# Kernel tuning notes

Hardware: AMD Instinct MI355X
Metric: run time of the kernel (lower is better)

Reference implementation:

```python
import jax, jax.numpy as jnp
import numpy as np

SMILE_LEN = 40


def _gru_cell(x, h, Wih, Whh, bih, bhh):
    # PyTorch GRU gate order: r, z, n
    gi = x @ Wih.T + bih          # [B, 3H]
    gh = h @ Whh.T + bhh          # [B, 3H]
    H = h.shape[-1]
    ir, iz, inn = gi[:, :H], gi[:, H:2 * H], gi[:, 2 * H:]
    hr, hz, hn = gh[:, :H], gh[:, H:2 * H], gh[:, 2 * H:]
    r = jax.nn.sigmoid(ir + hr)
    z = jax.nn.sigmoid(iz + hz)
    n = jnp.tanh(inn + r * hn)
    return (1.0 - z) * n + z * h


def setup_inputs() -> dict:
    key = jax.random.key(0)
    ks = jax.random.split(key, 12)
    B, L, H, A = 16384, 128, 256, 21
    s = 0.05
    return {
        "latent": jax.random.normal(ks[0], (B, L), jnp.float32),
        "W1": jax.random.normal(ks[1], (H, L), jnp.float32) * s,
        "b1": jax.random.normal(ks[2], (H,), jnp.float32) * s,
        "W2": jax.random.normal(ks[3], (H, H), jnp.float32) * s,
        "b2": jax.random.normal(ks[4], (H,), jnp.float32) * s,
        "Wih": jax.random.normal(ks[5], (3 * H, A), jnp.float32) * s,
        "Whh": jax.random.normal(ks[6], (3 * H, H), jnp.float32) * s,
        "bih": jax.random.normal(ks[7], (3 * H,), jnp.float32) * s,
        "bhh": jax.random.normal(ks[8], (3 * H,), jnp.float32) * s,
        "Wd": jax.random.normal(ks[9], (A, H), jnp.float32) * s,
        "bd": jax.random.normal(ks[10], (A,), jnp.float32) * s,
    }


def reference(latent, W1, b1, W2, b2, Wih, Whh, bih, bhh, Wd, bd):
    B = latent.shape[0]
    A = Wih.shape[1]
    # latent -> Dense -> ReLU -> (Dropout: identity in eval) -> Dense
    hidden = jax.nn.relu(latent @ W1.T + b1) @ W2.T + b2  # [B, H]
    # start token: +32 at position 0, -32 elsewhere
    start = jnp.full((B, A), -32.0, jnp.float32).at[:, 0].set(32.0)

    def step(carry, _):
        h, inp = carry
        h_new = _gru_cell(inp, h, Wih, Whh, bih, bhh)
        pred = h_new @ Wd.T + bd                      # [B, A]
        return (h_new, jax.lax.stop_gradient(pred)), pred

    (_, _), preds = jax.lax.scan(step, (hidden, start), None, length=SMILE_LEN - 1)
    # preds: [T-1, B, A] -> y: [B, T, A] with start token at t=0
    y = jnp.concatenate([start[:, None, :], jnp.transpose(preds, (1, 0, 2))], axis=1)
    return y
```

## Files before the change

kernel.cpp:

```cpp
#include <hip/hip_runtime.h>
#include <hip/hip_bf16.h>


typedef __bf16 bf16x8 __attribute__((ext_vector_type(8)));
typedef float  f32x16 __attribute__((ext_vector_type(16)));

#define MFMA32(a,b,c) __builtin_amdgcn_mfma_f32_32x32x16_bf16((a),(b),(c),0,0,0)

static constexpr int A_DIM = 21;

static constexpr size_t O_W1F   = 0;
static constexpr size_t O_W2F   = O_W1F  + 256*128*2;
static constexpr size_t O_WHHF  = O_W2F  + 256*256*2;
static constexpr size_t O_WMF   = O_WHHF + 768*256*2;
static constexpr size_t O_WDF   = O_WMF  + 1024*256*2;
static constexpr size_t O_BMAIN = O_WDF  + 32*256*2;
static constexpr size_t O_GI1   = O_BMAIN + 1024*4;


__global__ void prep_frag(const float* __restrict__ src, __bf16* __restrict__ dst,
                          int SR, int SC, int NF, int NCH) {
  int total = NF * NCH * 512;
  for (int i = blockIdx.x * blockDim.x + threadIdx.x; i < total;
       i += gridDim.x * blockDim.x) {
    int fragid = i >> 9;
    int within = i & 511;
    int lane = within >> 3, j = within & 7;
    int nf = fragid / NCH, kc = fragid - nf * NCH;
    int n = nf * 32 + (lane & 31);
    int k = kc * 16 + (lane >> 5) * 8 + j;
    float v = (n < SR && k < SC) ? src[n * SC + k] : 0.f;
    dst[i] = (__bf16)v;
  }
}

__global__ void prep_wmain(const float* __restrict__ Whh, const float* __restrict__ Wih,
                           const float* __restrict__ Wd, __bf16* __restrict__ dst) {
  int total = 32 * 16 * 512;
  for (int i = blockIdx.x * blockDim.x + threadIdx.x; i < total;
       i += gridDim.x * blockDim.x) {
    int fragid = i >> 9;
    int within = i & 511;
    int lane = within >> 3, j = within & 7;
    int nf = fragid >> 4, kc = fragid & 15;
    int n = nf * 32 + (lane & 31);
    int k = kc * 16 + (lane >> 5) * 8 + j;
    float v = 0.f;
    if (n < 768) v = Whh[n * 256 + k];
    if (n < 512 || n >= 768) {
      int nn = (n < 512) ? n : (n - 256);
      float d = 0.f;
      #pragma unroll
      for (int q = 0; q < A_DIM; ++q) d += Wih[nn * A_DIM + q] * Wd[q * 256 + k];
      v += d;
    }
    dst[i] = (__bf16)v;
  }
}

__global__ void prep_bias(const float* __restrict__ Wih, const float* __restrict__ bih,
                          const float* __restrict__ bhh, const float* __restrict__ bd,
                          float* __restrict__ bmain, float* __restrict__ gi1c) {
  int i = blockIdx.x * blockDim.x + threadIdx.x;
  if (i < 1024) {
    float bm;
    if (i < 512) {
      float d = 0.f;
      #pragma unroll
      for (int q = 0; q < A_DIM; ++q) d += Wih[i * A_DIM + q] * bd[q];
      bm = bhh[i] + bih[i] + d;
    } else if (i < 768) {
      bm = bhh[i];
    } else {
      int nn = i - 256;
      float d = 0.f;
      #pragma unroll
      for (int q = 0; q < A_DIM; ++q) d += Wih[nn * A_DIM + q] * bd[q];
      bm = bih[nn] + d;
    }
    bmain[i] = bm;
  }
  if (i < 768) {
    float s = 32.f * Wih[i * A_DIM + 0];
    #pragma unroll
    for (int q = 1; q < A_DIM; ++q) s -= 32.f * Wih[i * A_DIM + q];
    gi1c[i] = s + bih[i];
  }
}


__device__ __forceinline__ bf16x8 lds_frag(const __bf16* base, int rowBytes,
                                           int row, int kb) {
  return *(const bf16x8*)((const char*)base + row * rowBytes +
                          (kb ^ ((row & 7) << 4)));
}

__device__ __forceinline__ void gru_gate(const f32x16& ar, const f32x16& az,
                                         const f32x16& ah, const f32x16& ai,
                                         f32x16& hr) {
  #pragma unroll
  for (int g = 0; g < 16; ++g) {
    float r = __builtin_amdgcn_rcpf(1.f + __builtin_amdgcn_exp2f(ar[g] * -1.442695041f));
    float z = __builtin_amdgcn_rcpf(1.f + __builtin_amdgcn_exp2f(az[g] * -1.442695041f));
    float pre = ai[g] + r * ah[g];
    float e = __builtin_amdgcn_exp2f(pre * 2.885390082f);
    float n = 1.f - 2.f * __builtin_amdgcn_rcpf(e + 1.f);
    hr[g] = n + z * (hr[g] - n);
  }
}

__device__ __forceinline__ void write_h(__bf16* hl, int c, int hfv,
                                        const f32x16& hr0, const f32x16& hr1) {
  #pragma unroll
  for (int g = 0; g < 16; ++g) {
    int pat = (g & 3) + 8 * (g >> 2) + 4 * hfv;
    int sw = (2 * c) ^ ((pat & 7) << 4);
    *(__bf16*)((char*)hl + pat * 512 + sw)        = (__bf16)hr0[g];
    *(__bf16*)((char*)hl + (32 + pat) * 512 + sw) = (__bf16)hr1[g];
  }
}

__global__ __launch_bounds__(512, 2) void decoder_main(
    const float* __restrict__ latent, const float* __restrict__ b1,
    const float* __restrict__ b2, const float* __restrict__ bhh,
    const float* __restrict__ bd, const float* __restrict__ gi1c,
    const float* __restrict__ bmain,
    const __bf16* __restrict__ W1f, const __bf16* __restrict__ W2f,
    const __bf16* __restrict__ Whhf, const __bf16* __restrict__ Wmf,
    const __bf16* __restrict__ Wdf, float* __restrict__ y) {
  __shared__ __bf16 h_lds[64 * 256];
  __shared__ __bf16 h1_lds[64 * 256];
  __shared__ __bf16 lat_lds[64 * 128];

  const int tid = threadIdx.x;
  const int w = tid >> 6;
  const int l = tid & 63;
  const int lc = l & 31;
  const int hfv = l >> 5;
  const int b0 = blockIdx.x * 64;
  const int c = w * 32 + lc;

  for (int i = tid; i < 64 * A_DIM; i += 512) {
    int r = i / A_DIM, a = i - r * A_DIM;
    y[(size_t)(b0 + r) * 840 + a] = (a == 0) ? 32.f : -32.f;
  }

  for (int i = tid; i < 64 * 32; i += 512) {
    int r = i >> 5, c4 = i & 31;
    const float4 v = *(const float4*)(latent + (size_t)(b0 + r) * 128 + c4 * 4);
    __bf16* q = (__bf16*)((char*)lat_lds + r * 256 + ((c4 * 8) ^ ((r & 7) << 4)));
    q[0] = (__bf16)v.x; q[1] = (__bf16)v.y; q[2] = (__bf16)v.z; q[3] = (__bf16)v.w;
  }
  __syncthreads();

  const bf16x8* W1v = (const bf16x8*)W1f;
  const bf16x8* W2v = (const bf16x8*)W2f;
  const bf16x8* Whv = (const bf16x8*)Whhf;
  const bf16x8* Wmv = (const bf16x8*)Wmf;
  const bf16x8* Wdv = (const bf16x8*)Wdf;

  f32x16 acc0, acc1;
  {
    const float bb = b1[c];
    #pragma unroll
    for (int i = 0; i < 16; ++i) { acc0[i] = bb; acc1[i] = bb; }
  }
  #pragma unroll
  for (int kc = 0; kc < 8; ++kc) {
    bf16x8 a0 = lds_frag(lat_lds, 256, lc, kc * 32 + hfv * 16);
    bf16x8 a1 = lds_frag(lat_lds, 256, 32 + lc, kc * 32 + hfv * 16);
    bf16x8 bw = W1v[(w * 8 + kc) * 64 + l];
    acc0 = MFMA32(a0, bw, acc0);
    acc1 = MFMA32(a1, bw, acc1);
  }
  #pragma unroll
  for (int g = 0; g < 16; ++g) {
    int pat = (g & 3) + 8 * (g >> 2) + 4 * hfv;
    int sw = (2 * c) ^ ((pat & 7) << 4);
    float v0 = acc0[g] > 0.f ? acc0[g] : 0.f;
    float v1 = acc1[g] > 0.f ? acc1[g] : 0.f;
    *(__bf16*)((char*)h1_lds + pat * 512 + sw)        = (__bf16)v0;
    *(__bf16*)((char*)h1_lds + (32 + pat) * 512 + sw) = (__bf16)v1;
  }
  __syncthreads();

  f32x16 hr0, hr1;
  {
    const float bb = b2[c];
    #pragma unroll
    for (int i = 0; i < 16; ++i) { hr0[i] = bb; hr1[i] = bb; }
  }
  #pragma unroll
  for (int kc = 0; kc < 16; ++kc) {
    bf16x8 a0 = lds_frag(h1_lds, 512, lc, kc * 32 + hfv * 16);
    bf16x8 a1 = lds_frag(h1_lds, 512, 32 + lc, kc * 32 + hfv * 16);
    bf16x8 bw = W2v[(w * 16 + kc) * 64 + l];
    hr0 = MFMA32(a0, bw, hr0);
    hr1 = MFMA32(a1, bw, hr1);
  }
  write_h(h_lds, c, hfv, hr0, hr1);
  __syncthreads();

  const float i_r1 = bhh[c] + gi1c[c];
  const float i_z1 = bhh[256 + c] + gi1c[256 + c];
  const float i_h1 = bhh[512 + c];
  const float i_n1 = gi1c[512 + c];
  const float i_rm = bmain[c];
  const float i_zm = bmain[256 + c];
  const float i_hm = bmain[512 + c];
  const float i_nm = bmain[768 + c];
  const float pb = (lc < A_DIM) ? bd[lc] : 0.f;

  f32x16 aR0, aR1, aZ0, aZ1, aH0, aH1, aI0, aI1, pacc;

  {
    #pragma unroll
    for (int i = 0; i < 16; ++i) {
      aR0[i] = i_r1; aR1[i] = i_r1; aZ0[i] = i_z1; aZ1[i] = i_z1;
      aH0[i] = i_h1; aH1[i] = i_h1; aI0[i] = i_n1; aI1[i] = i_n1;
    }
    const bf16x8* Wr = Whv + (size_t)(w) * 16 * 64;
    const bf16x8* Wz = Whv + (size_t)(8 + w) * 16 * 64;
    const bf16x8* Wh = Whv + (size_t)(16 + w) * 16 * 64;
    #pragma unroll
    for (int kc = 0; kc < 16; ++kc) {
      bf16x8 a0 = lds_frag(h_lds, 512, lc, kc * 32 + hfv * 16);
      bf16x8 a1 = lds_frag(h_lds, 512, 32 + lc, kc * 32 + hfv * 16);
      bf16x8 br = Wr[kc * 64 + l];
      bf16x8 bz = Wz[kc * 64 + l];
      bf16x8 bh = Wh[kc * 64 + l];
      aR0 = MFMA32(a0, br, aR0); aR1 = MFMA32(a1, br, aR1);
      aZ0 = MFMA32(a0, bz, aZ0); aZ1 = MFMA32(a1, bz, aZ1);
      aH0 = MFMA32(a0, bh, aH0); aH1 = MFMA32(a1, bh, aH1);
    }
    gru_gate(aR0, aZ0, aH0, aI0, hr0);
    gru_gate(aR1, aZ1, aH1, aI1, hr1);
    __syncthreads();
    write_h(h_lds, c, hfv, hr0, hr1);
    __syncthreads();
  }

  const bf16x8* Wr = Wmv + (size_t)(w) * 16 * 64;
  const bf16x8* Wz = Wmv + (size_t)(8 + w) * 16 * 64;
  const bf16x8* Wh = Wmv + (size_t)(16 + w) * 16 * 64;
  const bf16x8* Wi = Wmv + (size_t)(24 + w) * 16 * 64;
  #pragma unroll 1
  for (int t = 2; t <= 39; ++t) {
    #pragma unroll
    for (int i = 0; i < 16; ++i) {
      aR0[i] = i_rm; aR1[i] = i_rm; aZ0[i] = i_zm; aZ1[i] = i_zm;
      aH0[i] = i_hm; aH1[i] = i_hm; aI0[i] = i_nm; aI1[i] = i_nm;
      pacc[i] = pb;
    }
    #pragma unroll
    for (int kc = 0; kc < 16; ++kc) {
      bf16x8 a0 = lds_frag(h_lds, 512, lc, kc * 32 + hfv * 16);
      bf16x8 a1 = lds_frag(h_lds, 512, 32 + lc, kc * 32 + hfv * 16);
      bf16x8 br = Wr[kc * 64 + l];
      bf16x8 bz = Wz[kc * 64 + l];
      bf16x8 bh = Wh[kc * 64 + l];
      bf16x8 bi = Wi[kc * 64 + l];
      aR0 = MFMA32(a0, br, aR0); aR1 = MFMA32(a1, br, aR1);
      aZ0 = MFMA32(a0, bz, aZ0); aZ1 = MFMA32(a1, bz, aZ1);
      aH0 = MFMA32(a0, bh, aH0); aH1 = MFMA32(a1, bh, aH1);
      aI0 = MFMA32(a0, bi, aI0); aI1 = MFMA32(a1, bi, aI1);
      if (w < 2) {
        bf16x8 bp = Wdv[kc * 64 + l];
        pacc = MFMA32(w ? a1 : a0, bp, pacc);
      }
    }
    if (w < 2 && lc < A_DIM) {
      #pragma unroll
      for (int g = 0; g < 16; ++g) {
        int pat = (g & 3) + 8 * (g >> 2) + 4 * hfv;
        y[(size_t)(b0 + 32 * w + pat) * 840 + (size_t)(t - 1) * 21 + lc] = pacc[g];
      }
    }
    gru_gate(aR0, aZ0, aH0, aI0, hr0);
    gru_gate(aR1, aZ1, aH1, aI1, hr1);
    __syncthreads();
    write_h(h_lds, c, hfv, hr0, hr1);
    __syncthreads();
  }

  if (w < 2) {
    #pragma unroll
    for (int i = 0; i < 16; ++i) pacc[i] = pb;
    #pragma unroll
    for (int kc = 0; kc < 16; ++kc) {
      bf16x8 a = lds_frag(h_lds, 512, 32 * w + lc, kc * 32 + hfv * 16);
      bf16x8 bp = Wdv[kc * 64 + l];
      pacc = MFMA32(a, bp, pacc);
    }
    if (lc < A_DIM) {
      #pragma unroll
      for (int g = 0; g < 16; ++g) {
        int pat = (g & 3) + 8 * (g >> 2) + 4 * hfv;
        y[(size_t)(b0 + 32 * w + pat) * 840 + 39 * 21 + lc] = pacc[g];
      }
    }
  }
}

extern "C" void kernel_launch(void* const* d_in, const int* in_sizes, int n_in,
                              void* d_out, int out_size, void* d_ws, size_t ws_size,
                              hipStream_t stream) {
  const float* latent = (const float*)d_in[0];
  const float* W1 = (const float*)d_in[1];
  const float* b1 = (const float*)d_in[2];
  const float* W2 = (const float*)d_in[3];
  const float* b2 = (const float*)d_in[4];
  const float* Wih = (const float*)d_in[5];
  const float* Whh = (const float*)d_in[6];
  const float* bih = (const float*)d_in[7];
  const float* bhh = (const float*)d_in[8];
  const float* Wd = (const float*)d_in[9];
  const float* bd = (const float*)d_in[10];
  float* y = (float*)d_out;
  char* ws = (char*)d_ws;

  __bf16* W1f = (__bf16*)(ws + O_W1F);
  __bf16* W2f = (__bf16*)(ws + O_W2F);
  __bf16* Whhf = (__bf16*)(ws + O_WHHF);
  __bf16* Wmf = (__bf16*)(ws + O_WMF);
  __bf16* Wdf = (__bf16*)(ws + O_WDF);
  float* bmain = (float*)(ws + O_BMAIN);
  float* gi1c = (float*)(ws + O_GI1);

  prep_frag<<<128, 256, 0, stream>>>(W1, W1f, 256, 128, 8, 8);
  prep_frag<<<256, 256, 0, stream>>>(W2, W2f, 256, 256, 8, 16);
  prep_frag<<<512, 256, 0, stream>>>(Whh, Whhf, 768, 256, 24, 16);
  prep_frag<<<32, 256, 0, stream>>>(Wd, Wdf, 21, 256, 1, 16);
  prep_wmain<<<1024, 256, 0, stream>>>(Whh, Wih, Wd, Wmf);
  prep_bias<<<4, 256, 0, stream>>>(Wih, bih, bhh, bd, bmain, gi1c);

  decoder_main<<<256, 512, 0, stream>>>(latent, b1, b2, bhh, bd, gi1c, bmain,
                                        W1f, W2f, Whhf, Wmf, Wdf, y);
}
```

Measured before the change: 1.649 ms.

## Stream recurrent weights through an LDS ring buffer with async global-to-LDS loads

The GRU weight fragments are re-laid out per wave into interleaved slices (r, z, h, i gates plus the Wd projection) and prefetched two k-chunks ahead into a triple-buffered per-wave LDS ring using global_load_lds. This replaces direct per-lane global vector loads inside the MFMA loop and is meant to hide global and L2 latency behind the matrix ops. The __syncthreads calls become manual lgkmcnt waits plus s_barrier so that in-flight vmem prefetches stay outstanding across timesteps. The LDS footprint changes and the hand-counted vmcnt waits are fragile, and LDS use could limit the two-blocks-per-CU occupancy.

```diff
diff --git a/kernel.cpp b/kernel.cpp
--- a/kernel.cpp
+++ b/kernel.cpp
@@ -6,15 +6,17 @@
 typedef float  f32x16 __attribute__((ext_vector_type(16)));
 
 #define MFMA32(a,b,c) __builtin_amdgcn_mfma_f32_32x32x16_bf16((a),(b),(c),0,0,0)
+#define WAITV(n) asm volatile("s_waitcnt vmcnt(" #n ")" ::: "memory")
+#define LGKM0()  asm volatile("s_waitcnt lgkmcnt(0)" ::: "memory")
+#define BARRIER() do { asm volatile("" ::: "memory"); __builtin_amdgcn_s_barrier(); asm volatile("" ::: "memory"); } while (0)
 
 static constexpr int A_DIM = 21;
 
 static constexpr size_t O_W1F   = 0;
-static constexpr size_t O_W2F   = O_W1F  + 256*128*2;
-static constexpr size_t O_WHHF  = O_W2F  + 256*256*2;
-static constexpr size_t O_WMF   = O_WHHF + 768*256*2;
-static constexpr size_t O_WDF   = O_WMF  + 1024*256*2;
-static constexpr size_t O_BMAIN = O_WDF  + 32*256*2;
+static constexpr size_t O_W2F   = O_W1F + 256*128*2;
+static constexpr size_t O_ST1   = O_W2F + 256*256*2;
+static constexpr size_t O_WMN   = O_ST1 + 8*16*3*1024;
+static constexpr size_t O_BMAIN = O_WMN + 8*16*5*1024;
 static constexpr size_t O_GI1   = O_BMAIN + 1024*4;
 
 
@@ -23,8 +25,7 @@
   int total = NF * NCH * 512;
   for (int i = blockIdx.x * blockDim.x + threadIdx.x; i < total;
        i += gridDim.x * blockDim.x) {
-    int fragid = i >> 9;
-    int within = i & 511;
+    int fragid = i >> 9, within = i & 511;
     int lane = within >> 3, j = within & 7;
     int nf = fragid / NCH, kc = fragid - nf * NCH;
     int n = nf * 32 + (lane & 31);
@@ -34,25 +35,42 @@
   }
 }
 
-__global__ void prep_wmain(const float* __restrict__ Whh, const float* __restrict__ Wih,
-                           const float* __restrict__ Wd, __bf16* __restrict__ dst) {
-  int total = 32 * 16 * 512;
+__global__ void prep_st1(const float* __restrict__ Whh, __bf16* __restrict__ dst) {
+  int total = 8 * 16 * 3 * 512;
   for (int i = blockIdx.x * blockDim.x + threadIdx.x; i < total;
        i += gridDim.x * blockDim.x) {
-    int fragid = i >> 9;
-    int within = i & 511;
-    int lane = within >> 3, j = within & 7;
-    int nf = fragid >> 4, kc = fragid & 15;
-    int n = nf * 32 + (lane & 31);
+    int j = i & 7, lane = (i >> 3) & 63;
+    int slice = i >> 9;
+    int g = slice % 3, kc = (slice / 3) & 15, w = slice / 48;
+    int n = g * 256 + w * 32 + (lane & 31);
+    int k = kc * 16 + (lane >> 5) * 8 + j;
+    dst[i] = (__bf16)Whh[n * 256 + k];
+  }
+}
+
+__global__ void prep_main(const float* __restrict__ Whh, const float* __restrict__ Wih,
+                          const float* __restrict__ Wd, __bf16* __restrict__ dst) {
+  int total = 8 * 16 * 5 * 512;
+  for (int i = blockIdx.x * blockDim.x + threadIdx.x; i < total;
+       i += gridDim.x * blockDim.x) {
+    int j = i & 7, lane = (i >> 3) & 63;
+    int slice = i >> 9;
+    int g = slice % 5, kc = (slice / 5) & 15, w = slice / 80;
     int k = kc * 16 + (lane >> 5) * 8 + j;
     float v = 0.f;
-    if (n < 768) v = Whh[n * 256 + k];
-    if (n < 512 || n >= 768) {
-      int nn = (n < 512) ? n : (n - 256);
-      float d = 0.f;
-      #pragma unroll
-      for (int q = 0; q < A_DIM; ++q) d += Wih[nn * A_DIM + q] * Wd[q * 256 + k];
-      v += d;
+    if (g == 4) {
+      int n = lane & 31;
+      v = (n < A_DIM) ? Wd[n * 256 + k] : 0.f;
+    } else {
+      int n = g * 256 + w * 32 + (lane & 31);
+      if (n < 768) v = Whh[n * 256 + k];
+      if (n < 512 || n >= 768) {
+        int nn = (n < 512) ? n : (n - 256);
+        float d = 0.f;
+        #pragma unroll
+        for (int q = 0; q < A_DIM; ++q) d += Wih[nn * A_DIM + q] * Wd[q * 256 + k];
+        v += d;
+      }
     }
     dst[i] = (__bf16)v;
   }
@@ -89,6 +107,11 @@
 }
 
 
+__device__ __forceinline__ void gload16(const void* g, void* l) {
+  __builtin_amdgcn_global_load_lds((const __attribute__((address_space(1))) void*)g,
+                                   (__attribute__((address_space(3))) void*)l, 16, 0, 0);
+}
+
 __device__ __forceinline__ bf16x8 lds_frag(const __bf16* base, int rowBytes,
                                            int row, int kb) {
   return *(const bf16x8*)((const char*)base + row * rowBytes +
@@ -126,11 +149,10 @@
     const float* __restrict__ bd, const float* __restrict__ gi1c,
     const float* __restrict__ bmain,
     const __bf16* __restrict__ W1f, const __bf16* __restrict__ W2f,
-    const __bf16* __restrict__ Whhf, const __bf16* __restrict__ Wmf,
-    const __bf16* __restrict__ Wdf, float* __restrict__ y) {
-  __shared__ __bf16 h_lds[64 * 256];
-  __shared__ __bf16 h1_lds[64 * 256];
-  __shared__ __bf16 lat_lds[64 * 128];
+    const __bf16* __restrict__ St1, const __bf16* __restrict__ Wmn,
+    float* __restrict__ y) {
+  __shared__ __attribute__((aligned(16))) __bf16 h_lds[64 * 256];
+  __shared__ __attribute__((aligned(16))) char ringmem[8 * 3 * 5120];
 
   const int tid = threadIdx.x;
   const int w = tid >> 6;
@@ -140,6 +162,9 @@
   const int b0 = blockIdx.x * 64;
   const int c = w * 32 + lc;
 
+  __bf16* lat_al = (__bf16*)(ringmem);
+  __bf16* h1_al  = (__bf16*)(ringmem + 16384);
+
   for (int i = tid; i < 64 * A_DIM; i += 512) {
     int r = i / A_DIM, a = i - r * A_DIM;
     y[(size_t)(b0 + r) * 840 + a] = (a == 0) ? 32.f : -32.f;
@@ -148,16 +173,13 @@
   for (int i = tid; i < 64 * 32; i += 512) {
     int r = i >> 5, c4 = i & 31;
     const float4 v = *(const float4*)(latent + (size_t)(b0 + r) * 128 + c4 * 4);
-    __bf16* q = (__bf16*)((char*)lat_lds + r * 256 + ((c4 * 8) ^ ((r & 7) << 4)));
+    __bf16* q = (__bf16*)((char*)lat_al + r * 256 + ((c4 * 8) ^ ((r & 7) << 4)));
     q[0] = (__bf16)v.x; q[1] = (__bf16)v.y; q[2] = (__bf16)v.z; q[3] = (__bf16)v.w;
   }
   __syncthreads();
 
   const bf16x8* W1v = (const bf16x8*)W1f;
   const bf16x8* W2v = (const bf16x8*)W2f;
-  const bf16x8* Whv = (const bf16x8*)Whhf;
-  const bf16x8* Wmv = (const bf16x8*)Wmf;
-  const bf16x8* Wdv = (const bf16x8*)Wdf;
 
   f32x16 acc0, acc1;
   {
@@ -167,8 +189,8 @@
   }
   #pragma unroll
   for (int kc = 0; kc < 8; ++kc) {
-    bf16x8 a0 = lds_frag(lat_lds, 256, lc, kc * 32 + hfv * 16);
-    bf16x8 a1 = lds_frag(lat_lds, 256, 32 + lc, kc * 32 + hfv * 16);
+    bf16x8 a0 = lds_frag(lat_al, 256, lc, kc * 32 + hfv * 16);
+    bf16x8 a1 = lds_frag(lat_al, 256, 32 + lc, kc * 32 + hfv * 16);
     bf16x8 bw = W1v[(w * 8 + kc) * 64 + l];
     acc0 = MFMA32(a0, bw, acc0);
     acc1 = MFMA32(a1, bw, acc1);
@@ -179,8 +201,8 @@
     int sw = (2 * c) ^ ((pat & 7) << 4);
     float v0 = acc0[g] > 0.f ? acc0[g] : 0.f;
     float v1 = acc1[g] > 0.f ? acc1[g] : 0.f;
-    *(__bf16*)((char*)h1_lds + pat * 512 + sw)        = (__bf16)v0;
-    *(__bf16*)((char*)h1_lds + (32 + pat) * 512 + sw) = (__bf16)v1;
+    *(__bf16*)((char*)h1_al + pat * 512 + sw)        = (__bf16)v0;
+    *(__bf16*)((char*)h1_al + (32 + pat) * 512 + sw) = (__bf16)v1;
   }
   __syncthreads();
 
@@ -192,8 +214,8 @@
   }
   #pragma unroll
   for (int kc = 0; kc < 16; ++kc) {
-    bf16x8 a0 = lds_frag(h1_lds, 512, lc, kc * 32 + hfv * 16);
-    bf16x8 a1 = lds_frag(h1_lds, 512, 32 + lc, kc * 32 + hfv * 16);
+    bf16x8 a0 = lds_frag(h1_al, 512, lc, kc * 32 + hfv * 16);
+    bf16x8 a1 = lds_frag(h1_al, 512, 32 + lc, kc * 32 + hfv * 16);
     bf16x8 bw = W2v[(w * 16 + kc) * 64 + l];
     hr0 = MFMA32(a0, bw, hr0);
     hr1 = MFMA32(a1, bw, hr1);
@@ -211,39 +233,58 @@
   const float i_nm = bmain[768 + c];
   const float pb = (lc < A_DIM) ? bd[lc] : 0.f;
 
+  char* ringw = ringmem + w * 15360;
+  const char* sW1 = (const char*)St1 + w * 49152 + (size_t)l * 16;
+  const char* sW  = (const char*)Wmn + w * 81920 + (size_t)l * 16;
+
   f32x16 aR0, aR1, aZ0, aZ1, aH0, aH1, aI0, aI1, pacc;
 
-  {
-    #pragma unroll
-    for (int i = 0; i < 16; ++i) {
-      aR0[i] = i_r1; aR1[i] = i_r1; aZ0[i] = i_z1; aZ1[i] = i_z1;
-      aH0[i] = i_h1; aH1[i] = i_h1; aI0[i] = i_n1; aI1[i] = i_n1;
-    }
-    const bf16x8* Wr = Whv + (size_t)(w) * 16 * 64;
-    const bf16x8* Wz = Whv + (size_t)(8 + w) * 16 * 64;
-    const bf16x8* Wh = Whv + (size_t)(16 + w) * 16 * 64;
-    #pragma unroll
-    for (int kc = 0; kc < 16; ++kc) {
-      bf16x8 a0 = lds_frag(h_lds, 512, lc, kc * 32 + hfv * 16);
-      bf16x8 a1 = lds_frag(h_lds, 512, 32 + lc, kc * 32 + hfv * 16);
-      bf16x8 br = Wr[kc * 64 + l];
-      bf16x8 bz = Wz[kc * 64 + l];
-      bf16x8 bh = Wh[kc * 64 + l];
-      aR0 = MFMA32(a0, br, aR0); aR1 = MFMA32(a1, br, aR1);
-      aZ0 = MFMA32(a0, bz, aZ0); aZ1 = MFMA32(a1, bz, aZ1);
-      aH0 = MFMA32(a0, bh, aH0); aH1 = MFMA32(a1, bh, aH1);
-    }
-    gru_gate(aR0, aZ0, aH0, aI0, hr0);
-    gru_gate(aR1, aZ1, aH1, aI1, hr1);
-    __syncthreads();
-    write_h(h_lds, c, hfv, hr0, hr1);
-    __syncthreads();
-  }
-
-  const bf16x8* Wr = Wmv + (size_t)(w) * 16 * 64;
-  const bf16x8* Wz = Wmv + (size_t)(8 + w) * 16 * 64;
-  const bf16x8* Wh = Wmv + (size_t)(16 + w) * 16 * 64;
-  const bf16x8* Wi = Wmv + (size_t)(24 + w) * 16 * 64;
+  #pragma unroll
+  for (int p = 0; p < 2; ++p)
+    #pragma unroll
+    for (int g = 0; g < 3; ++g)
+      gload16(sW1 + p * 3072 + g * 1024, ringw + p * 5120 + g * 1024);
+
+  #pragma unroll
+  for (int i = 0; i < 16; ++i) {
+    aR0[i] = i_r1; aR1[i] = i_r1; aZ0[i] = i_z1; aZ1[i] = i_z1;
+    aH0[i] = i_h1; aH1[i] = i_h1; aI0[i] = i_n1; aI1[i] = i_n1;
+  }
+  #pragma unroll
+  for (int kc = 0; kc < 16; ++kc) {
+    if (kc < 14) {
+      const int fi = (kc + 2) % 3;
+      #pragma unroll
+      for (int g = 0; g < 3; ++g)
+        gload16(sW1 + (kc + 2) * 3072 + g * 1024, ringw + fi * 5120 + g * 1024);
+    }
+    if (kc < 14) { WAITV(6); } else if (kc == 14) { WAITV(3); } else { WAITV(0); }
+    const char* fc = ringw + (kc % 3) * 5120 + (size_t)l * 16;
+    bf16x8 a0 = lds_frag(h_lds, 512, lc, kc * 32 + hfv * 16);
+    bf16x8 a1 = lds_frag(h_lds, 512, 32 + lc, kc * 32 + hfv * 16);
+    bf16x8 br = *(const bf16x8*)(fc);
+    bf16x8 bz = *(const bf16x8*)(fc + 1024);
+    bf16x8 bh = *(const bf16x8*)(fc + 2048);
+    aR0 = MFMA32(a0, br, aR0); aR1 = MFMA32(a1, br, aR1);
+    aZ0 = MFMA32(a0, bz, aZ0); aZ1 = MFMA32(a1, bz, aZ1);
+    aH0 = MFMA32(a0, bh, aH0); aH1 = MFMA32(a1, bh, aH1);
+  }
+
+  #pragma unroll
+  for (int p = 0; p < 2; ++p) {
+    #pragma unroll
+    for (int g = 0; g < 4; ++g)
+      gload16(sW + p * 5120 + g * 1024, ringw + p * 5120 + g * 1024);
+    if (w < 2) gload16(sW + p * 5120 + 4096, ringw + p * 5120 + 4096);
+  }
+
+  gru_gate(aR0, aZ0, aH0, aI0, hr0);
+  gru_gate(aR1, aZ1, aH1, aI1, hr1);
+  LGKM0(); BARRIER();
+  write_h(h_lds, c, hfv, hr0, hr1);
+  LGKM0(); BARRIER();
+
+  int base = 0;
   #pragma unroll 1
   for (int t = 2; t <= 39; ++t) {
     #pragma unroll
@@ -254,18 +295,31 @@
     }
     #pragma unroll
     for (int kc = 0; kc < 16; ++kc) {
+      {
+        int f2 = (kc + 2) % 3 + base; if (f2 >= 3) f2 -= 3;
+        const char* gsrc = sW + ((kc + 2) & 15) * 5120;
+        char* fd = ringw + f2 * 5120;
+        gload16(gsrc,        fd);
+        gload16(gsrc + 1024, fd + 1024);
+        gload16(gsrc + 2048, fd + 2048);
+        gload16(gsrc + 3072, fd + 3072);
+        if (w < 2) gload16(gsrc + 4096, fd + 4096);
+      }
+      WAITV(8);
+      int f0i = kc % 3 + base; if (f0i >= 3) f0i -= 3;
+      const char* fc = ringw + f0i * 5120 + (size_t)l * 16;
       bf16x8 a0 = lds_frag(h_lds, 512, lc, kc * 32 + hfv * 16);
       bf16x8 a1 = lds_frag(h_lds, 512, 32 + lc, kc * 32 + hfv * 16);
-      bf16x8 br = Wr[kc * 64 + l];
-      bf16x8 bz = Wz[kc * 64 + l];
-      bf16x8 bh = Wh[kc * 64 + l];
-      bf16x8 bi = Wi[kc * 64 + l];
+      bf16x8 br = *(const bf16x8*)(fc);
+      bf16x8 bz = *(const bf16x8*)(fc + 1024);
+      bf16x8 bh = *(const bf16x8*)(fc + 2048);
+      bf16x8 bi = *(const bf16x8*)(fc + 3072);
       aR0 = MFMA32(a0, br, aR0); aR1 = MFMA32(a1, br, aR1);
       aZ0 = MFMA32(a0, bz, aZ0); aZ1 = MFMA32(a1, bz, aZ1);
       aH0 = MFMA32(a0, bh, aH0); aH1 = MFMA32(a1, bh, aH1);
       aI0 = MFMA32(a0, bi, aI0); aI1 = MFMA32(a1, bi, aI1);
       if (w < 2) {
-        bf16x8 bp = Wdv[kc * 64 + l];
+        bf16x8 bp = *(const bf16x8*)(fc + 4096);
         pacc = MFMA32(w ? a1 : a0, bp, pacc);
       }
     }
@@ -278,9 +332,10 @@
     }
     gru_gate(aR0, aZ0, aH0, aI0, hr0);
     gru_gate(aR1, aZ1, aH1, aI1, hr1);
-    __syncthreads();
+    LGKM0(); BARRIER();
     write_h(h_lds, c, hfv, hr0, hr1);
-    __syncthreads();
+    LGKM0(); BARRIER();
+    base = (base == 2) ? 0 : base + 1;
   }
 
   if (w < 2) {
@@ -289,7 +344,8 @@
     #pragma unroll
     for (int kc = 0; kc < 16; ++kc) {
       bf16x8 a = lds_frag(h_lds, 512, 32 * w + lc, kc * 32 + hfv * 16);
-      bf16x8 bp = Wdv[kc * 64 + l];
+      bf16x8 bp = *(const bf16x8*)((const char*)Wmn + (size_t)(kc * 5 + 4) * 1024 +
+                                   (size_t)l * 16);
       pacc = MFMA32(a, bp, pacc);
     }
     if (lc < A_DIM) {
@@ -300,6 +356,7 @@
       }
     }
   }
+  WAITV(0);
 }
 
 extern "C" void kernel_launch(void* const* d_in, const int* in_sizes, int n_in,
@@ -321,19 +378,17 @@
 
   __bf16* W1f = (__bf16*)(ws + O_W1F);
   __bf16* W2f = (__bf16*)(ws + O_W2F);
-  __bf16* Whhf = (__bf16*)(ws + O_WHHF);
-  __bf16* Wmf = (__bf16*)(ws + O_WMF);
-  __bf16* Wdf = (__bf16*)(ws + O_WDF);
+  __bf16* St1 = (__bf16*)(ws + O_ST1);
+  __bf16* Wmn = (__bf16*)(ws + O_WMN);
   float* bmain = (float*)(ws + O_BMAIN);
   float* gi1c = (float*)(ws + O_GI1);
 
   prep_frag<<<128, 256, 0, stream>>>(W1, W1f, 256, 128, 8, 8);
   prep_frag<<<256, 256, 0, stream>>>(W2, W2f, 256, 256, 8, 16);
-  prep_frag<<<512, 256, 0, stream>>>(Whh, Whhf, 768, 256, 24, 16);
-  prep_frag<<<32, 256, 0, stream>>>(Wd, Wdf, 21, 256, 1, 16);
-  prep_wmain<<<1024, 256, 0, stream>>>(Whh, Wih, Wd, Wmf);
+  prep_st1<<<512, 256, 0, stream>>>(Whh, St1);
+  prep_main<<<1024, 256, 0, stream>>>(Whh, Wih, Wd, Wmn);
   prep_bias<<<4, 256, 0, stream>>>(Wih, bih, bhh, bd, bmain, gi1c);
 
   decoder_main<<<256, 512, 0, stream>>>(latent, b1, b2, bhh, bd, gi1c, bmain,
-                                        W1f, W2f, Whhf, Wmf, Wdf, y);
-}
+                                        W1f, W2f, St1, Wmn, y);
+}
```

Result: faster. 1.450 ms (-12.1%).
